# Kernel tuning notes

Hardware: AMD Instinct MI355X
Metric: run time of the kernel (lower is better)

Reference implementation:

```python
import jax, jax.numpy as jnp
import numpy as np

B, Q, D, H, HD = 16, 300, 256, 8, 32
LV, P, NL, FF, NC = 3, 4, 6, 1024, 80
SPATIAL = ((80, 80), (40, 40), (20, 20))
LEN = sum(h * w for h, w in SPATIAL)  # 8400


def _layer_norm(x, g, b):
    m = jnp.mean(x, -1, keepdims=True)
    v = jnp.mean((x - m) ** 2, -1, keepdims=True)
    return (x - m) * jax.lax.rsqrt(v + 1e-5) * g + b


def _inverse_sigmoid(x, eps=1e-5):
    x = jnp.clip(x, eps, 1.0 - eps)
    return jnp.log(x / (1.0 - x))


def _bilinear(img, x, y, Hl, Wl):
    # img: (B*H, C, Hl*Wl); x, y: (B*H, N) pixel coords; matches
    # F.grid_sample(align_corners=False, padding_mode='zeros')
    x0 = jnp.floor(x)
    y0 = jnp.floor(y)
    wx1 = x - x0
    wy1 = y - y0

    def g(xi, yi, w):
        valid = (xi >= 0) & (xi <= Wl - 1) & (yi >= 0) & (yi <= Hl - 1)
        idx = jnp.clip(yi, 0, Hl - 1).astype(jnp.int32) * Wl + jnp.clip(xi, 0, Wl - 1).astype(jnp.int32)
        idxb = jnp.broadcast_to(idx[:, None, :], (img.shape[0], img.shape[1], idx.shape[-1]))
        v = jnp.take_along_axis(img, idxb, axis=2)
        return v * (w * valid)[:, None, :]

    return (g(x0, y0, (1 - wx1) * (1 - wy1)) + g(x0 + 1, y0, wx1 * (1 - wy1))
            + g(x0, y0 + 1, (1 - wx1) * wy1) + g(x0 + 1, y0 + 1, wx1 * wy1))


def _msda(query, ref, value, oW, ob, aW, ab, OW, Ob):
    # query: (B,Q,D); ref: (B,Q,4) in [0,1]; value: (B,LEN,H,HD)
    off = (query @ oW + ob).reshape(B, Q, H, LV, P, 2)
    aw = jax.nn.softmax((query @ aW + ab).reshape(B, Q, H, LV * P), -1).reshape(B, Q, H, LV, P)
    loc = ref[:, :, None, None, None, :2] + off / P * ref[:, :, None, None, None, 2:] * 0.5
    out = jnp.zeros((B, Q, H, HD), query.dtype)
    start = 0
    for l, (Hl, Wl) in enumerate(SPATIAL):
        img = value[:, start:start + Hl * Wl].transpose(0, 2, 3, 1).reshape(B * H, HD, Hl * Wl)
        start += Hl * Wl
        gl = loc[:, :, :, l].transpose(0, 2, 1, 3, 4).reshape(B * H, Q * P, 2)
        s = _bilinear(img, gl[..., 0] * Wl - 0.5, gl[..., 1] * Hl - 0.5, Hl, Wl).reshape(B, H, HD, Q, P)
        out = out + jnp.einsum('bhdqp,bqhp->bqhd', s, aw[:, :, :, l])
    return out.reshape(B, Q, D) @ OW + Ob


def _mha(qx, kx, vx, Wq, bq, Wk, bk, Wv, bv, Wo, bo):
    q = (qx @ Wq + bq).reshape(B, Q, H, HD)
    k = (kx @ Wk + bk).reshape(B, Q, H, HD)
    v = (vx @ Wv + bv).reshape(B, Q, H, HD)
    a = jax.nn.softmax(jnp.einsum('bqhd,bkhd->bhqk', q, k) * np.float32(1.0 / np.sqrt(HD)), -1)
    return jnp.einsum('bhqk,bkhd->bqhd', a, v).reshape(B, Q, D) @ Wo + bo


def _core(tgt, ref_points_unact, memory, self_Wq, self_bq, self_Wk, self_bk, self_Wv, self_bv, self_Wo, self_bo, ln1_g, ln1_b, ln2_g, ln2_b, ln3_g, ln3_b, off_W, off_b, aw_W, aw_b, val_W, val_b, out_W, out_b, ffn_W1, ffn_b1, ffn_W2, ffn_b2, qph_W1, qph_b1, qph_W2, qph_b2, bb_W1, bb_b1, bb_W2, bb_b2, bb_W3, bb_b3, sc_W, sc_b):
    out = tgt
    ref = jax.nn.sigmoid(ref_points_unact)
    for i in range(NL):
        qpe = jax.nn.relu(ref @ qph_W1 + qph_b1) @ qph_W2 + qph_b2
        q = out + qpe
        out = _layer_norm(out + _mha(q, q, out, self_Wq[i], self_bq[i], self_Wk[i], self_bk[i], self_Wv[i], self_bv[i], self_Wo[i], self_bo[i]), ln1_g[i], ln1_b[i])
        value = (memory @ val_W[i] + val_b[i]).reshape(B, LEN, H, HD)
        out = _layer_norm(out + _msda(out + qpe, ref, value, off_W[i], off_b[i], aw_W[i], aw_b[i], out_W[i], out_b[i]), ln2_g[i], ln2_b[i])
        ff = jax.nn.relu(out @ ffn_W1[i] + ffn_b1[i]) @ ffn_W2[i] + ffn_b2[i]
        out = _layer_norm(out + ff, ln3_g[i], ln3_b[i])
        bb = jax.nn.relu(out @ bb_W1[i] + bb_b1[i])
        bb = jax.nn.relu(bb @ bb_W2[i] + bb_b2[i])
        bb = bb @ bb_W3[i] + bb_b3[i]
        ref = jax.nn.sigmoid(bb + _inverse_sigmoid(ref))
    logits = out @ sc_W[NL - 1] + sc_b[NL - 1]
    return ref, logits


def setup_inputs():
    ks = iter(jax.random.split(jax.random.key(0), 48))

    def rn(shape, s=0.02):
        return jax.random.normal(next(ks), shape, jnp.float32) * s

    z = lambda shape: jnp.zeros(shape, jnp.float32)
    o = lambda shape: jnp.ones(shape, jnp.float32)
    L = NL
    return {
        'tgt': rn((B, Q, D), 1.0),
        'ref_points_unact': rn((B, Q, 4), 1.0),
        'memory': rn((B, LEN, D), 1.0),
        'memory_spatial_shapes': jnp.array(SPATIAL, jnp.int32),
        'self_Wq': rn((L, D, D)), 'self_bq': z((L, D)),
        'self_Wk': rn((L, D, D)), 'self_bk': z((L, D)),
        'self_Wv': rn((L, D, D)), 'self_bv': z((L, D)),
        'self_Wo': rn((L, D, D)), 'self_bo': z((L, D)),
        'ln1_g': o((L, D)), 'ln1_b': z((L, D)),
        'ln2_g': o((L, D)), 'ln2_b': z((L, D)),
        'ln3_g': o((L, D)), 'ln3_b': z((L, D)),
        'off_W': rn((L, D, H * LV * P * 2)), 'off_b': rn((L, H * LV * P * 2), 0.5),
        'aw_W': rn((L, D, H * LV * P)), 'aw_b': z((L, H * LV * P)),
        'val_W': rn((L, D, D)), 'val_b': z((L, D)),
        'out_W': rn((L, D, D)), 'out_b': z((L, D)),
        'ffn_W1': rn((L, D, FF)), 'ffn_b1': z((L, FF)),
        'ffn_W2': rn((L, FF, D)), 'ffn_b2': z((L, D)),
        'qph_W1': rn((4, 2 * D)), 'qph_b1': z((2 * D,)),
        'qph_W2': rn((2 * D, D)), 'qph_b2': z((D,)),
        'bb_W1': rn((L, D, D)), 'bb_b1': z((L, D)),
        'bb_W2': rn((L, D, D)), 'bb_b2': z((L, D)),
        'bb_W3': rn((L, D, 4)), 'bb_b3': z((L, 4)),
        'sc_W': rn((L, D, NC)), 'sc_b': z((L, NC)),
    }


def reference(tgt, ref_points_unact, memory, memory_spatial_shapes, self_Wq, self_bq, self_Wk, self_bk, self_Wv, self_bv, self_Wo, self_bo, ln1_g, ln1_b, ln2_g, ln2_b, ln3_g, ln3_b, off_W, off_b, aw_W, aw_b, val_W, val_b, out_W, out_b, ffn_W1, ffn_b1, ffn_W2, ffn_b2, qph_W1, qph_b1, qph_W2, qph_b2, bb_W1, bb_b1, bb_W2, bb_b2, bb_W3, bb_b3, sc_W, sc_b):
    # memory_spatial_shapes must equal SPATIAL (static constants under jit)
    ref, logits = _core(tgt, ref_points_unact, memory, self_Wq, self_bq, self_Wk, self_bk, self_Wv, self_bv, self_Wo, self_bo, ln1_g, ln1_b, ln2_g, ln2_b, ln3_g, ln3_b, off_W, off_b, aw_W, aw_b, val_W, val_b, out_W, out_b, ffn_W1, ffn_b1, ffn_W2, ffn_b2, qph_W1, qph_b1, qph_W2, qph_b2, bb_W1, bb_b1, bb_W2, bb_b2, bb_W3, bb_b3, sc_W, sc_b)
    # eval path: stacked outputs from the eval_idx (last) layer
    return (ref[None], logits[None])
```

## Files before the change

kernel.cpp:

```cpp
#include <hip/hip_runtime.h>

#define DI __device__ __forceinline__

typedef __attribute__((ext_vector_type(8))) short short8;
typedef __attribute__((ext_vector_type(4))) float f32x4;
typedef unsigned short u16;

DI u16 f2bf(float f) {
    union { float f; unsigned u; } v; v.f = f;
    unsigned u = v.u;
    return (u16)((u + 0x7fffu + ((u >> 16) & 1u)) >> 16);
}
DI float bf2f(u16 h) {
    union { unsigned u; float f; } v; v.u = ((unsigned)h) << 16;
    return v.f;
}
DI int lds_off(int row, int slot) {
    return row * 64 + (((slot ^ ((row >> 1) & 3)) << 4));
}

__global__ __launch_bounds__(256) void k_wt(const float* __restrict__ W, u16* __restrict__ Wt,
                                            int K, int N, int dstL)
{
    __shared__ u16 t[32][33];
    const int tid = threadIdx.x;
    const int kt = blockIdx.x * 32, nt = blockIdx.y * 32;
    const float* Wl = W + (size_t)blockIdx.z * K * N;
    u16* Wtl = Wt + (size_t)blockIdx.z * dstL;
#pragma unroll
    for (int i = 0; i < 4; i++) {
        int k = kt + (tid >> 5) + i * 8;
        int n = nt + (tid & 31);
        float v = (n < N) ? Wl[(size_t)k * N + n] : 0.f;
        t[tid & 31][(tid >> 5) + i * 8] = f2bf(v);
    }
    __syncthreads();
#pragma unroll
    for (int i = 0; i < 4; i++) {
        int n = nt + (tid >> 5) + i * 8;
        int k = kt + (tid & 31);
        if (n < N) Wtl[(size_t)n * K + k] = t[(tid >> 5) + i * 8][tid & 31];
    }
}

__global__ void k_packbias(const float* __restrict__ a, const float* __restrict__ b,
                           int na, int nb, float* __restrict__ dst)
{
    int i = blockIdx.x * 256 + threadIdx.x;
    int L = blockIdx.z;
    float* d = dst + (size_t)L * (na + nb);
    if (i < na) d[i] = a[(size_t)L * na + i];
    if (i < nb) d[na + i] = b[(size_t)L * nb + i];
}

template<int TM, int AMODE, int STORE, bool RELU, bool RESID>
__global__ __launch_bounds__(256) void k_gemm(
    const void* __restrict__ Ap, const float* __restrict__ A2,
    const u16* __restrict__ Bt, const float* __restrict__ bias,
    const float* __restrict__ resid, void* __restrict__ Cp,
    int M, int N, int K)
{
    constexpr int MI = TM / 32;
    __shared__ alignas(16) char Asm[TM * 64];
    __shared__ alignas(16) char Bsm[128 * 64];
    const int tid  = threadIdx.x;
    const int lane = tid & 63;
    const int wave = tid >> 6;
    const int wr = wave >> 1, wc = wave & 1;
    const int m0 = blockIdx.x * TM, n0 = blockIdx.y * 128;

    f32x4 acc[MI][4] = {};

    for (int kb = 0; kb < K; kb += 32) {
        if (AMODE == 2) {
            const u16* A = (const u16*)Ap;
            int r = tid >> 2, ko = (tid & 3) << 3;
            int grow = m0 + r; if (grow > M - 1) grow = M - 1;
            uint4 v = *(const uint4*)(A + (size_t)grow * K + kb + ko);
            *(uint4*)(Asm + lds_off(r, ko >> 3)) = v;
        } else {
            constexpr int AIT = (TM * 8) / 256;
#pragma unroll
            for (int j = 0; j < AIT; j++) {
                int flat = tid + j * 256;
                int r = flat >> 3, kq = flat & 7;
                int grow = m0 + r; if (grow > M - 1) grow = M - 1;
                const float* p = (const float*)Ap + (size_t)grow * K + kb + (kq << 2);
                float4 v = *(const float4*)p;
                if (AMODE == 1) {
                    float4 w = *(const float4*)(A2 + (size_t)grow * K + kb + (kq << 2));
                    v.x += w.x; v.y += w.y; v.z += w.z; v.w += w.w;
                }
                ushort4 h; h.x = f2bf(v.x); h.y = f2bf(v.y); h.z = f2bf(v.z); h.w = f2bf(v.w);
                *(ushort4*)(Asm + lds_off(r, kq >> 1) + ((kq & 1) << 3)) = h;
            }
        }
#pragma unroll
        for (int j = 0; j < 2; j++) {
            int item = tid + j * 256;
            int n = item >> 2, kq = item & 3;
            int gn = n0 + n; if (gn > N - 1) gn = N - 1;
            uint4 v = *(const uint4*)(Bt + (size_t)gn * K + kb + (kq << 3));
            *(uint4*)(Bsm + lds_off(n, kq)) = v;
        }
        __syncthreads();

        short8 af[MI], bfr[4];
#pragma unroll
        for (int mi = 0; mi < MI; mi++) {
            int r = wr * (TM / 2) + (mi << 4) + (lane & 15);
            af[mi] = *(const short8*)(Asm + lds_off(r, lane >> 4));
        }
#pragma unroll
        for (int ni = 0; ni < 4; ni++) {
            int c = (wc << 6) + (ni << 4) + (lane & 15);
            bfr[ni] = *(const short8*)(Bsm + lds_off(c, lane >> 4));
        }
#pragma unroll
        for (int mi = 0; mi < MI; mi++)
#pragma unroll
            for (int ni = 0; ni < 4; ni++)
                acc[mi][ni] = __builtin_amdgcn_mfma_f32_16x16x32_bf16(af[mi], bfr[ni], acc[mi][ni], 0, 0, 0);
        __syncthreads();
    }

    const int cl = lane & 15, rb = (lane >> 4) << 2;
#pragma unroll
    for (int mi = 0; mi < MI; mi++) {
#pragma unroll
        for (int ni = 0; ni < 4; ni++) {
            int col = n0 + (wc << 6) + (ni << 4) + cl;
            if (col >= N) continue;
            float bv = bias[col];
#pragma unroll
            for (int e = 0; e < 4; e++) {
                int row = m0 + wr * (TM / 2) + (mi << 4) + rb + e;
                if (row >= M) continue;
                float v = acc[mi][ni][e] + bv;
                if (RESID) v += resid[(size_t)row * N + col];
                if (RELU)  v = fmaxf(v, 0.f);
                if (STORE == 0) {
                    ((float*)Cp)[(size_t)row * N + col] = v;
                } else {
                    int b = row / 8400, pix = row - b * 8400;
                    int h = col >> 5, hd = col & 31;
                    ((u16*)Cp)[(((size_t)(b * 8 + h)) * 8400 + pix) * 32 + hd] = f2bf(v);
                }
            }
        }
    }
}

__global__ __launch_bounds__(320) void k_mha2(const float* __restrict__ qk, const float* __restrict__ Vp,
                                              float* __restrict__ outp)
{
    __shared__ float Ksh[300 * 32];
    __shared__ u16   Vsh[300 * 32];
    const int qt = blockIdx.x & 3;
    const int bh = blockIdx.x >> 2;
    const int h = bh & 7, b = bh >> 3;
    const float scale = 0.17677669529663687f;

    for (int i = threadIdx.x; i < 9600; i += 320) {
        int kk = i >> 5, dd = i & 31;
        size_t row = (size_t)(b * 300 + kk);
        Ksh[i] = qk[row * 512 + 256 + h * 32 + dd] * scale;
        Vsh[i] = f2bf(Vp[row * 256 + h * 32 + dd]);
    }
    __syncthreads();

    const int qq = threadIdx.x >> 2;
    const int quarter = threadIdx.x & 3;
    int q = qt * 75 + qq; if (q > 299) q = 299;
    const float* qg = qk + (size_t)(b * 300 + q) * 512 + h * 32 + quarter * 8;
    float qv[8];
    {
        float4 q0 = *(const float4*)qg, q1 = *(const float4*)(qg + 4);
        qv[0]=q0.x; qv[1]=q0.y; qv[2]=q0.z; qv[3]=q0.w;
        qv[4]=q1.x; qv[5]=q1.y; qv[6]=q1.z; qv[7]=q1.w;
    }

    float mx = -1e30f;
    for (int kk = 0; kk < 300; kk++) {
        const float* kr = Ksh + kk * 32 + quarter * 8;
        float4 k0 = *(const float4*)kr, k1 = *(const float4*)(kr + 4);
        float s = qv[0]*k0.x + qv[1]*k0.y + qv[2]*k0.z + qv[3]*k0.w
                + qv[4]*k1.x + qv[5]*k1.y + qv[6]*k1.z + qv[7]*k1.w;
        s += __shfl_xor(s, 1);
        s += __shfl_xor(s, 2);
        mx = fmaxf(mx, s);
    }
    float l = 0.f;
    float acc[8];
#pragma unroll
    for (int j = 0; j < 8; j++) acc[j] = 0.f;
    for (int kk = 0; kk < 300; kk++) {
        const float* kr = Ksh + kk * 32 + quarter * 8;
        float4 k0 = *(const float4*)kr, k1 = *(const float4*)(kr + 4);
        float s = qv[0]*k0.x + qv[1]*k0.y + qv[2]*k0.z + qv[3]*k0.w
                + qv[4]*k1.x + qv[5]*k1.y + qv[6]*k1.z + qv[7]*k1.w;
        s += __shfl_xor(s, 1);
        s += __shfl_xor(s, 2);
        float p = __expf(s - mx);
        l += p;
        uint4 vv = *(const uint4*)(Vsh + kk * 32 + quarter * 8);
        acc[0] += p * bf2f((u16)(vv.x & 0xffff));
        acc[1] += p * bf2f((u16)(vv.x >> 16));
        acc[2] += p * bf2f((u16)(vv.y & 0xffff));
        acc[3] += p * bf2f((u16)(vv.y >> 16));
        acc[4] += p * bf2f((u16)(vv.z & 0xffff));
        acc[5] += p * bf2f((u16)(vv.z >> 16));
        acc[6] += p * bf2f((u16)(vv.w & 0xffff));
        acc[7] += p * bf2f((u16)(vv.w >> 16));
    }
    if (qq < 75) {
        float inv = 1.f / l;
        float* op = outp + (size_t)(b * 300 + qt * 75 + qq) * 256 + h * 32 + quarter * 8;
        float4 o0, o1;
        o0.x = acc[0]*inv; o0.y = acc[1]*inv; o0.z = acc[2]*inv; o0.w = acc[3]*inv;
        o1.x = acc[4]*inv; o1.y = acc[5]*inv; o1.z = acc[6]*inv; o1.w = acc[7]*inv;
        *(float4*)op = o0;
        *(float4*)(op + 4) = o1;
    }
}

__global__ __launch_bounds__(256) void k_ln(const float* __restrict__ x, const float* __restrict__ g,
                                            const float* __restrict__ bb, float* __restrict__ out, int M)
{
    int row = blockIdx.x * 4 + (threadIdx.x >> 6);
    int lane = threadIdx.x & 63;
    if (row >= M) return;
    const float* xr = x + (size_t)row * 256;
    float4 v = *(const float4*)(xr + lane * 4);
    float s  = v.x + v.y + v.z + v.w;
    float s2 = v.x*v.x + v.y*v.y + v.z*v.z + v.w*v.w;
#pragma unroll
    for (int off = 32; off >= 1; off >>= 1) {
        s  += __shfl_xor(s, off);
        s2 += __shfl_xor(s2, off);
    }
    float m   = s * 0.00390625f;
    float var = s2 * 0.00390625f - m * m;
    float r   = rsqrtf(var + 1e-5f);
    float4 gv = *(const float4*)(g + lane * 4);
    float4 bv = *(const float4*)(bb + lane * 4);
    float4 o;
    o.x = (v.x - m) * r * gv.x + bv.x;
    o.y = (v.y - m) * r * gv.y + bv.y;
    o.z = (v.z - m) * r * gv.z + bv.z;
    o.w = (v.w - m) * r * gv.w + bv.w;
    *(float4*)(out + (size_t)row * 256 + lane * 4) = o;
}

__global__ void k_awsm(float* __restrict__ offaw, int n)
{
    int g = blockIdx.x * 256 + threadIdx.x;
    if (g >= n) return;
    int row = g >> 3, h = g & 7;
    float* p = offaw + (size_t)row * 288 + 192 + h * 12;
    float m = p[0];
#pragma unroll
    for (int i = 1; i < 12; i++) m = fmaxf(m, p[i]);
    float e[12]; float s = 0.f;
#pragma unroll
    for (int i = 0; i < 12; i++) { e[i] = __expf(p[i] - m); s += e[i]; }
    float inv = 1.f / s;
#pragma unroll
    for (int i = 0; i < 12; i++) p[i] = e[i] * inv;
}

__global__ __launch_bounds__(256) void k_msda(const u16* __restrict__ value, const float* __restrict__ offaw,
                                              const float* __restrict__ ref, float* __restrict__ samp)
{
    int it = blockIdx.x * 8 + (threadIdx.x >> 5);
    int d  = threadIdx.x & 31;
    int h = it & 7, row = it >> 3;
    int b = row / 300;
    const float* rf = ref + (size_t)row * 4;
    float rx = rf[0], ry = rf[1];
    float rw = rf[2] * 0.125f, rh = rf[3] * 0.125f;
    const float* offp = offaw + (size_t)row * 288 + h * 24;
    const float* awp  = offaw + (size_t)row * 288 + 192 + h * 12;
    const u16* vb = value + ((size_t)(b * 8 + h)) * 8400 * 32 + d;
    const int HW[3] = {80, 40, 20};
    const int st[3] = {0, 6400, 8000};
    float acc = 0.f;
#pragma unroll
    for (int lv = 0; lv < 3; lv++) {
        int Wl = HW[lv], Hl = HW[lv];
        float Wf = (float)Wl, Hf = (float)Hl;
#pragma unroll
        for (int p = 0; p < 4; p++) {
            float a = awp[lv * 4 + p];
            float x = (rx + offp[lv*8 + p*2]     * rw) * Wf - 0.5f;
            float y = (ry + offp[lv*8 + p*2 + 1] * rh) * Hf - 0.5f;
            float xf = floorf(x), yf = floorf(y);
            float wx = x - xf, wy = y - yf;
            int x0 = (int)xf, y0 = (int)yf;
#pragma unroll
            for (int t = 0; t < 4; t++) {
                int xx = x0 + (t & 1), yy = y0 + (t >> 1);
                if (xx >= 0 && xx < Wl && yy >= 0 && yy < Hl) {
                    float w = ((t & 1) ? wx : 1.f - wx) * ((t >> 1) ? wy : 1.f - wy);
                    acc += a * w * bf2f(vb[(size_t)(st[lv] + yy * Wl + xx) * 32]);
                }
            }
        }
    }
    samp[(size_t)row * 256 + h * 32 + d] = acc;
}

__global__ void k_qpe_hidden(const float* __restrict__ ref, const float* __restrict__ W1,
                             const float* __restrict__ b1, float* __restrict__ hid)
{
    int idx = blockIdx.x * 256 + threadIdx.x;
    if (idx >= 4800 * 512) return;
    int row = idx >> 9, col = idx & 511;
    const float* r = ref + (size_t)row * 4;
    float v = b1[col] + r[0]*W1[col] + r[1]*W1[512+col] + r[2]*W1[1024+col] + r[3]*W1[1536+col];
    hid[idx] = fmaxf(v, 0.f);
}

__global__ __launch_bounds__(64) void k_bb3(const float* __restrict__ bb2, const float* __restrict__ W3,
                                            const float* __restrict__ b3, float* __restrict__ ref)
{
    int row = blockIdx.x;
    int lane = threadIdx.x;
    const float* xr = bb2 + (size_t)row * 256;
    float s0 = 0, s1 = 0, s2 = 0, s3 = 0;
#pragma unroll
    for (int k = lane; k < 256; k += 64) {
        float xv = xr[k];
        float4 w = *(const float4*)(W3 + k * 4);
        s0 += xv * w.x; s1 += xv * w.y; s2 += xv * w.z; s3 += xv * w.w;
    }
#pragma unroll
    for (int off = 32; off >= 1; off >>= 1) {
        s0 += __shfl_xor(s0, off); s1 += __shfl_xor(s1, off);
        s2 += __shfl_xor(s2, off); s3 += __shfl_xor(s3, off);
    }
    if (lane == 0) {
        float sv[4] = {s0, s1, s2, s3};
        float* rr = ref + (size_t)row * 4;
#pragma unroll
        for (int j = 0; j < 4; j++) {
            float v = sv[j] + b3[j];
            float o = rr[j];
            o = fminf(fmaxf(o, 1e-5f), 1.f - 1e-5f);
            float inv = logf(o / (1.f - o));
            rr[j] = 1.f / (1.f + expf(-(v + inv)));
        }
    }
}

__global__ void k_cvt_bf16(const float* __restrict__ in, u16* __restrict__ out, int n4)
{
    int i = blockIdx.x * 256 + threadIdx.x;
    if (i >= n4) return;
    float4 v = ((const float4*)in)[i];
    ushort4 h; h.x = f2bf(v.x); h.y = f2bf(v.y); h.z = f2bf(v.z); h.w = f2bf(v.w);
    ((ushort4*)out)[i] = h;
}
__global__ void k_copy4(const float* __restrict__ in, float* __restrict__ out, int n4)
{
    int i = blockIdx.x * 256 + threadIdx.x;
    if (i >= n4) return;
    ((float4*)out)[i] = ((const float4*)in)[i];
}
__global__ void k_sigmoid(const float* __restrict__ in, float* __restrict__ out, int n)
{
    int i = blockIdx.x * 256 + threadIdx.x;
    if (i >= n) return;
    out[i] = 1.f / (1.f + __expf(-in[i]));
}

static inline dim3 g32(int M, int N) { return dim3((M + 31) / 32, (N + 127) / 128); }

static void gemm_plain(const float* A, const u16* Bt, const float* bias, float* C,
                       int M, int N, int K, hipStream_t s) {
    k_gemm<32, 0, 0, false, false><<<g32(M, N), 256, 0, s>>>((const void*)A, nullptr, Bt, bias, nullptr, (void*)C, M, N, K);
}
static void gemm_add(const float* A, const float* A2, const u16* Bt, const float* bias, float* C,
                     int M, int N, int K, hipStream_t s) {
    k_gemm<32, 1, 0, false, false><<<g32(M, N), 256, 0, s>>>((const void*)A, A2, Bt, bias, nullptr, (void*)C, M, N, K);
}
static void gemm_resid(const float* A, const u16* Bt, const float* bias, const float* resid, float* C,
                       int M, int N, int K, hipStream_t s) {
    k_gemm<32, 0, 0, false, true><<<g32(M, N), 256, 0, s>>>((const void*)A, nullptr, Bt, bias, resid, (void*)C, M, N, K);
}
static void gemm_relu(const float* A, const u16* Bt, const float* bias, float* C,
                      int M, int N, int K, hipStream_t s) {
    k_gemm<32, 0, 0, true, false><<<g32(M, N), 256, 0, s>>>((const void*)A, nullptr, Bt, bias, nullptr, (void*)C, M, N, K);
}
static void gemm_value(const u16* A, const u16* Bt, const float* bias, u16* C, hipStream_t s) {
    k_gemm<64, 2, 1, false, false><<<dim3(2100, 2), 256, 0, s>>>((const void*)A, nullptr, Bt, bias, nullptr, (void*)C, 134400, 256, 256);
}

extern "C" void kernel_launch(void* const* d_in, const int* in_sizes, int n_in,
                              void* d_out, int out_size, void* d_ws, size_t ws_size,
                              hipStream_t stream)
{
    const float* tgt       = (const float*)d_in[0];
    const float* ref_unact = (const float*)d_in[1];
    const float* memory    = (const float*)d_in[2];
    const float* self_Wq = (const float*)d_in[4];
    const float* self_bq = (const float*)d_in[5];
    const float* self_Wk = (const float*)d_in[6];
    const float* self_bk = (const float*)d_in[7];
    const float* self_Wv = (const float*)d_in[8];
    const float* self_bv = (const float*)d_in[9];
    const float* self_Wo = (const float*)d_in[10];
    const float* self_bo = (const float*)d_in[11];
    const float* ln1_g = (const float*)d_in[12];
    const float* ln1_b = (const float*)d_in[13];
    const float* ln2_g = (const float*)d_in[14];
    const float* ln2_b = (const float*)d_in[15];
    const float* ln3_g = (const float*)d_in[16];
    const float* ln3_b = (const float*)d_in[17];
    const float* off_W = (const float*)d_in[18];
    const float* off_b = (const float*)d_in[19];
    const float* aw_W  = (const float*)d_in[20];
    const float* aw_b  = (const float*)d_in[21];
    const float* val_W = (const float*)d_in[22];
    const float* val_b = (const float*)d_in[23];
    const float* out_W = (const float*)d_in[24];
    const float* out_b = (const float*)d_in[25];
    const float* ffn_W1 = (const float*)d_in[26];
    const float* ffn_b1 = (const float*)d_in[27];
    const float* ffn_W2 = (const float*)d_in[28];
    const float* ffn_b2 = (const float*)d_in[29];
    const float* qph_W1 = (const float*)d_in[30];
    const float* qph_b1 = (const float*)d_in[31];
    const float* qph_W2 = (const float*)d_in[32];
    const float* qph_b2 = (const float*)d_in[33];
    const float* bb_W1 = (const float*)d_in[34];
    const float* bb_b1 = (const float*)d_in[35];
    const float* bb_W2 = (const float*)d_in[36];
    const float* bb_b2 = (const float*)d_in[37];
    const float* bb_W3 = (const float*)d_in[38];
    const float* bb_b3 = (const float*)d_in[39];
    const float* sc_W  = (const float*)d_in[40];
    const float* sc_b  = (const float*)d_in[41];
    float* out_f = (float*)d_out;

    char* w = (char*)d_ws;
    u16* mem_bf = (u16*)(w + 0);
    u16* value  = (u16*)(w + 68812800);
    const size_t F0 = 137625600;
    float* ws_out   = (float*)(w + F0);
    float* ws_tmp   = (float*)(w + F0 +  4915200);
    float* ws_qpe   = (float*)(w + F0 +  9830400);
    float* ws_hid   = (float*)(w + F0 + 14745600);
    float* ws_qk    = (float*)(w + F0 + 24576000);
    float* ws_v     = (float*)(w + F0 + 34406400);
    float* ws_attn  = (float*)(w + F0 + 39321600);
    float* ws_offaw = (float*)(w + F0 + 44236800);
    float* ws_samp  = (float*)(w + F0 + 49766400);
    float* ws_ffn   = (float*)(w + F0 + 54681600);
    float* ws_bb1   = (float*)(w + F0 + 74342400);
    float* ws_bb2   = (float*)(w + F0 + 79257600);
    float* ws_ref   = (float*)(w + F0 + 84172800);
    float* bias_qk  = (float*)(w + F0 + 84256800);
    float* bias_oa  = (float*)(w + F0 + 84269088);
    u16* wt = (u16*)(w + F0 + 84276000);
    u16* wt_qk    = wt;
    u16* wt_v     = wt_qk    + 786432;
    u16* wt_o     = wt_v     + 393216;
    u16* wt_offaw = wt_o     + 393216;
    u16* wt_val   = wt_offaw + 442368;
    u16* wt_out   = wt_val   + 393216;
    u16* wt_f1    = wt_out   + 393216;
    u16* wt_f2    = wt_f1    + 1572864;
    u16* wt_b1    = wt_f2    + 1572864;
    u16* wt_b2    = wt_b1    + 393216;
    u16* wt_qp2   = wt_b2    + 393216;
    u16* wt_sc    = wt_qp2   + 131072;

    k_wt<<<dim3(8, 8, 6),  256, 0, stream>>>(self_Wq, wt_qk,            256, 256, 131072);
    k_wt<<<dim3(8, 8, 6),  256, 0, stream>>>(self_Wk, wt_qk + 65536,    256, 256, 131072);
    k_wt<<<dim3(8, 8, 6),  256, 0, stream>>>(self_Wv, wt_v,             256, 256, 65536);
    k_wt<<<dim3(8, 8, 6),  256, 0, stream>>>(self_Wo, wt_o,             256, 256, 65536);
    k_wt<<<dim3(8, 6, 6),  256, 0, stream>>>(off_W,   wt_offaw,         256, 192, 73728);
    k_wt<<<dim3(8, 3, 6),  256, 0, stream>>>(aw_W,    wt_offaw + 49152, 256, 96,  73728);
    k_wt<<<dim3(8, 8, 6),  256, 0, stream>>>(val_W,   wt_val,           256, 256, 65536);
    k_wt<<<dim3(8, 8, 6),  256, 0, stream>>>(out_W,   wt_out,           256, 256, 65536);
    k_wt<<<dim3(8, 32, 6), 256, 0, stream>>>(ffn_W1,  wt_f1,            256, 1024, 262144);
    k_wt<<<dim3(32, 8, 6), 256, 0, stream>>>(ffn_W2,  wt_f2,            1024, 256, 262144);
    k_wt<<<dim3(8, 8, 6),  256, 0, stream>>>(bb_W1,   wt_b1,            256, 256, 65536);
    k_wt<<<dim3(8, 8, 6),  256, 0, stream>>>(bb_W2,   wt_b2,            256, 256, 65536);
    k_wt<<<dim3(16, 8, 1), 256, 0, stream>>>(qph_W2,  wt_qp2,           512, 256, 131072);
    k_wt<<<dim3(8, 3, 1),  256, 0, stream>>>(sc_W + (size_t)5 * 20480, wt_sc, 256, 80, 20480);
    k_packbias<<<dim3(1, 1, 6), 256, 0, stream>>>(self_bq, self_bk, 256, 256, bias_qk);
    k_packbias<<<dim3(1, 1, 6), 256, 0, stream>>>(off_b, aw_b, 192, 96, bias_oa);

    k_cvt_bf16<<<33600, 256, 0, stream>>>(memory, mem_bf, 8601600);
    k_copy4   <<<1200,  256, 0, stream>>>(tgt, ws_out, 307200);
    k_sigmoid <<<75,    256, 0, stream>>>(ref_unact, ws_ref, 19200);

    for (int l = 0; l < 6; l++) {
        k_qpe_hidden<<<9600, 256, 0, stream>>>(ws_ref, qph_W1, qph_b1, ws_hid);
        gemm_plain(ws_hid, wt_qp2, qph_b2, ws_qpe, 4800, 256, 512, stream);

        gemm_add(ws_out, ws_qpe, wt_qk + (size_t)l * 131072, bias_qk + l * 512, ws_qk, 4800, 512, 256, stream);
        gemm_plain(ws_out, wt_v + (size_t)l * 65536, self_bv + l * 256, ws_v, 4800, 256, 256, stream);
        k_mha2<<<512, 320, 0, stream>>>(ws_qk, ws_v, ws_attn);
        gemm_resid(ws_attn, wt_o + (size_t)l * 65536, self_bo + l * 256, ws_out, ws_tmp, 4800, 256, 256, stream);
        k_ln<<<1200, 256, 0, stream>>>(ws_tmp, ln1_g + l * 256, ln1_b + l * 256, ws_out, 4800);

        gemm_value(mem_bf, wt_val + (size_t)l * 65536, val_b + l * 256, value, stream);

        gemm_add(ws_out, ws_qpe, wt_offaw + (size_t)l * 73728, bias_oa + l * 288, ws_offaw, 4800, 288, 256, stream);
        k_awsm<<<150, 256, 0, stream>>>(ws_offaw, 38400);
        k_msda<<<4800, 256, 0, stream>>>(value, ws_offaw, ws_ref, ws_samp);
        gemm_resid(ws_samp, wt_out + (size_t)l * 65536, out_b + l * 256, ws_out, ws_tmp, 4800, 256, 256, stream);
        k_ln<<<1200, 256, 0, stream>>>(ws_tmp, ln2_g + l * 256, ln2_b + l * 256, ws_out, 4800);

        gemm_relu(ws_out, wt_f1 + (size_t)l * 262144, ffn_b1 + l * 1024, ws_ffn, 4800, 1024, 256, stream);
        gemm_resid(ws_ffn, wt_f2 + (size_t)l * 262144, ffn_b2 + l * 256, ws_out, ws_tmp, 4800, 256, 1024, stream);
        k_ln<<<1200, 256, 0, stream>>>(ws_tmp, ln3_g + l * 256, ln3_b + l * 256, ws_out, 4800);

        gemm_relu(ws_out, wt_b1 + (size_t)l * 65536, bb_b1 + l * 256, ws_bb1, 4800, 256, 256, stream);
        gemm_relu(ws_bb1, wt_b2 + (size_t)l * 65536, bb_b2 + l * 256, ws_bb2, 4800, 256, 256, stream);
        k_bb3<<<4800, 64, 0, stream>>>(ws_bb2, bb_W3 + (size_t)l * 1024, bb_b3 + l * 4, ws_ref);
    }

    k_copy4<<<19, 256, 0, stream>>>(ws_ref, out_f, 4800);
    gemm_plain(ws_out, wt_sc, sc_b + 5 * 80, out_f + 19200, 4800, 80, 256, stream);
}
```

Baseline: 2.733 ms.

## Rewrite self-attention kernel with bf16 MFMA for QK and PV

Replaces the scalar two-pass self-attention kernel with an MFMA-based one. Q and K are converted to bf16 and QK^T is computed with 16x16x32 MFMA into registers. Softmax is done in registers, and the probabilities are written to LDS that reuses the K region. V is transposed into LDS so PV also runs on MFMA. The goal is to remove the scalar FMA and shuffle cost of recomputing scores twice. The trade-offs are lower-precision scores (Q and K now in bf16), high register pressure from 19 accumulator tiles, and 640 blocks instead of 512.

```diff
diff --git a/kernel.cpp b/kernel.cpp
--- a/kernel.cpp
+++ b/kernel.cpp
@@ -151,76 +151,110 @@
     }
 }
 
-__global__ __launch_bounds__(320) void k_mha2(const float* __restrict__ qk, const float* __restrict__ Vp,
+__global__ __launch_bounds__(256) void k_mha3(const float* __restrict__ qk, const float* __restrict__ Vp,
                                               float* __restrict__ outp)
 {
-    __shared__ float Ksh[300 * 32];
-    __shared__ u16   Vsh[300 * 32];
-    const int qt = blockIdx.x & 3;
-    const int bh = blockIdx.x >> 2;
+    __shared__ alignas(16) char lds[62976];
+    u16* Ksh = (u16*)lds;
+    u16* Psh = (u16*)lds;
+    u16* Vt  = (u16*)(lds + 41984);
+
+    const int q0 = blockIdx.x * 64;
+    const int bh = blockIdx.y;
     const int h = bh & 7, b = bh >> 3;
+    const int tid = threadIdx.x;
+    const int wv = tid >> 6, l = tid & 63;
+    const int c15 = l & 15, slot = l >> 4;
     const float scale = 0.17677669529663687f;
 
-    for (int i = threadIdx.x; i < 9600; i += 320) {
-        int kk = i >> 5, dd = i & 31;
-        size_t row = (size_t)(b * 300 + kk);
-        Ksh[i] = qk[row * 512 + 256 + h * 32 + dd] * scale;
-        Vsh[i] = f2bf(Vp[row * 256 + h * 32 + dd]);
+    for (int item = tid; item < 304 * 8; item += 256) {
+        int kk = item >> 3, dq = (item & 7) << 2;
+        ushort4 hv = {0, 0, 0, 0};
+        if (kk < 300) {
+            float4 v = *(const float4*)(qk + (size_t)(b * 300 + kk) * 512 + 256 + h * 32 + dq);
+            hv.x = f2bf(v.x); hv.y = f2bf(v.y); hv.z = f2bf(v.z); hv.w = f2bf(v.w);
+        }
+        *(ushort4*)(Ksh + kk * 40 + dq) = hv;
+    }
+    for (int item = tid; item < 320 * 8; item += 256) {
+        int kk = item >> 3, dq = (item & 7) << 2;
+        float4 v = {0, 0, 0, 0};
+        if (kk < 300)
+            v = *(const float4*)(Vp + (size_t)(b * 300 + kk) * 256 + h * 32 + dq);
+        Vt[(dq + 0) * 328 + kk] = f2bf(v.x);
+        Vt[(dq + 1) * 328 + kk] = f2bf(v.y);
+        Vt[(dq + 2) * 328 + kk] = f2bf(v.z);
+        Vt[(dq + 3) * 328 + kk] = f2bf(v.w);
+    }
+    short8 qf;
+    {
+        int qrow = q0 + 16 * wv + c15; if (qrow > 299) qrow = 299;
+        const float* qs = qk + (size_t)(b * 300 + qrow) * 512 + h * 32 + (slot << 3);
+        float4 a0 = *(const float4*)qs, a1 = *(const float4*)(qs + 4);
+        qf[0] = (short)f2bf(a0.x * scale); qf[1] = (short)f2bf(a0.y * scale);
+        qf[2] = (short)f2bf(a0.z * scale); qf[3] = (short)f2bf(a0.w * scale);
+        qf[4] = (short)f2bf(a1.x * scale); qf[5] = (short)f2bf(a1.y * scale);
+        qf[6] = (short)f2bf(a1.z * scale); qf[7] = (short)f2bf(a1.w * scale);
     }
     __syncthreads();
 
-    const int qq = threadIdx.x >> 2;
-    const int quarter = threadIdx.x & 3;
-    int q = qt * 75 + qq; if (q > 299) q = 299;
-    const float* qg = qk + (size_t)(b * 300 + q) * 512 + h * 32 + quarter * 8;
-    float qv[8];
+    f32x4 sc[19];
+    const f32x4 zero4 = {0.f, 0.f, 0.f, 0.f};
+#pragma unroll
+    for (int t = 0; t < 19; t++) {
+        short8 kf = *(const short8*)(Ksh + (16 * t + c15) * 40 + (slot << 3));
+        sc[t] = __builtin_amdgcn_mfma_f32_16x16x32_bf16(qf, kf, zero4, 0, 0, 0);
+    }
+    __syncthreads();
+
+    float linv[4];
+    const int prow0 = 16 * wv + (slot << 2);
+#pragma unroll
+    for (int e = 0; e < 4; e++) {
+        float mm = -1e30f;
+#pragma unroll
+        for (int t = 0; t < 18; t++) mm = fmaxf(mm, sc[t][e]);
+        if (c15 < 12) mm = fmaxf(mm, sc[18][e]);
+        mm = fmaxf(mm, __shfl_xor(mm, 1));
+        mm = fmaxf(mm, __shfl_xor(mm, 2));
+        mm = fmaxf(mm, __shfl_xor(mm, 4));
+        mm = fmaxf(mm, __shfl_xor(mm, 8));
+        float ls = 0.f;
+#pragma unroll
+        for (int t = 0; t < 19; t++) {
+            float p = __expf(sc[t][e] - mm);
+            if (t == 18 && c15 >= 12) p = 0.f;
+            ls += p;
+            Psh[(prow0 + e) * 328 + 16 * t + c15] = f2bf(p);
+        }
+        ls += __shfl_xor(ls, 1);
+        ls += __shfl_xor(ls, 2);
+        ls += __shfl_xor(ls, 4);
+        ls += __shfl_xor(ls, 8);
+        linv[e] = 1.f / ls;
+    }
     {
-        float4 q0 = *(const float4*)qg, q1 = *(const float4*)(qg + 4);
-        qv[0]=q0.x; qv[1]=q0.y; qv[2]=q0.z; qv[3]=q0.w;
-        qv[4]=q1.x; qv[5]=q1.y; qv[6]=q1.z; qv[7]=q1.w;
-    }
-
-    float mx = -1e30f;
-    for (int kk = 0; kk < 300; kk++) {
-        const float* kr = Ksh + kk * 32 + quarter * 8;
-        float4 k0 = *(const float4*)kr, k1 = *(const float4*)(kr + 4);
-        float s = qv[0]*k0.x + qv[1]*k0.y + qv[2]*k0.z + qv[3]*k0.w
-                + qv[4]*k1.x + qv[5]*k1.y + qv[6]*k1.z + qv[7]*k1.w;
-        s += __shfl_xor(s, 1);
-        s += __shfl_xor(s, 2);
-        mx = fmaxf(mx, s);
-    }
-    float l = 0.f;
-    float acc[8];
-#pragma unroll
-    for (int j = 0; j < 8; j++) acc[j] = 0.f;
-    for (int kk = 0; kk < 300; kk++) {
-        const float* kr = Ksh + kk * 32 + quarter * 8;
-        float4 k0 = *(const float4*)kr, k1 = *(const float4*)(kr + 4);
-        float s = qv[0]*k0.x + qv[1]*k0.y + qv[2]*k0.z + qv[3]*k0.w
-                + qv[4]*k1.x + qv[5]*k1.y + qv[6]*k1.z + qv[7]*k1.w;
-        s += __shfl_xor(s, 1);
-        s += __shfl_xor(s, 2);
-        float p = __expf(s - mx);
-        l += p;
-        uint4 vv = *(const uint4*)(Vsh + kk * 32 + quarter * 8);
-        acc[0] += p * bf2f((u16)(vv.x & 0xffff));
-        acc[1] += p * bf2f((u16)(vv.x >> 16));
-        acc[2] += p * bf2f((u16)(vv.y & 0xffff));
-        acc[3] += p * bf2f((u16)(vv.y >> 16));
-        acc[4] += p * bf2f((u16)(vv.z & 0xffff));
-        acc[5] += p * bf2f((u16)(vv.z >> 16));
-        acc[6] += p * bf2f((u16)(vv.w & 0xffff));
-        acc[7] += p * bf2f((u16)(vv.w >> 16));
-    }
-    if (qq < 75) {
-        float inv = 1.f / l;
-        float* op = outp + (size_t)(b * 300 + qt * 75 + qq) * 256 + h * 32 + quarter * 8;
-        float4 o0, o1;
-        o0.x = acc[0]*inv; o0.y = acc[1]*inv; o0.z = acc[2]*inv; o0.w = acc[3]*inv;
-        o1.x = acc[4]*inv; o1.y = acc[5]*inv; o1.z = acc[6]*inv; o1.w = acc[7]*inv;
-        *(float4*)op = o0;
-        *(float4*)(op + 4) = o1;
+        int r = 16 * wv + (l >> 2);
+        int c = 304 + ((l & 3) << 2);
+        Psh[r * 328 + c + 0] = 0; Psh[r * 328 + c + 1] = 0;
+        Psh[r * 328 + c + 2] = 0; Psh[r * 328 + c + 3] = 0;
+    }
+
+#pragma unroll
+    for (int df = 0; df < 2; df++) {
+        f32x4 o = zero4;
+#pragma unroll
+        for (int t = 0; t < 10; t++) {
+            short8 pf = *(const short8*)(Psh + (16 * wv + c15) * 328 + 32 * t + (slot << 3));
+            short8 vf = *(const short8*)(Vt + (16 * df + c15) * 328 + 32 * t + (slot << 3));
+            o = __builtin_amdgcn_mfma_f32_16x16x32_bf16(pf, vf, o, 0, 0, 0);
+        }
+#pragma unroll
+        for (int e = 0; e < 4; e++) {
+            int qrow = q0 + prow0 + e;
+            if (qrow < 300)
+                outp[(size_t)(b * 300 + qrow) * 256 + h * 32 + 16 * df + c15] = o[e] * linv[e];
+        }
     }
 }
 
@@ -503,7 +537,7 @@
 
         gemm_add(ws_out, ws_qpe, wt_qk + (size_t)l * 131072, bias_qk + l * 512, ws_qk, 4800, 512, 256, stream);
         gemm_plain(ws_out, wt_v + (size_t)l * 65536, self_bv + l * 256, ws_v, 4800, 256, 256, stream);
-        k_mha2<<<512, 320, 0, stream>>>(ws_qk, ws_v, ws_attn);
+        k_mha3<<<dim3(5, 128), 256, 0, stream>>>(ws_qk, ws_v, ws_attn);
         gemm_resid(ws_attn, wt_o + (size_t)l * 65536, self_bo + l * 256, ws_out, ws_tmp, 4800, 256, 256, stream);
         k_ln<<<1200, 256, 0, stream>>>(ws_tmp, ln1_g + l * 256, ln1_b + l * 256, ws_out, 4800);
 
```

Result: faster. 2.208 ms (-19.2%).
